# Kernel optimization log

Hardware: AMD Instinct MI355X
Metric: run time of the kernel (lower is better)

Reference implementation:

```python
import jax, jax.numpy as jnp
import numpy as np
from functools import partial

VOCAB = 32000
EMBED = 512
HIDDEN = 1024
NUM_LAYERS = 2
REP_PENALTY = 1.2
BATCH, SEQ = 64, 128


def _lstm_layer(xs, w_ih, w_hh, b_ih, b_hh):
    """PyTorch-convention LSTM layer. xs: [B,T,D_in] -> hs: [B,T,H].
    Gate order i,f,g,o; weights [4H, D_in]/[4H, H]."""
    B = xs.shape[0]
    H = w_hh.shape[1]
    # precompute input projections for all timesteps: [B,T,4H]
    x_proj = jnp.einsum('btd,gd->btg', xs, w_ih) + b_ih + b_hh

    def step(carry, xp):
        h, c = carry
        gates = xp + h @ w_hh.T  # [B,4H]
        i, f, g, o = jnp.split(gates, 4, axis=-1)
        i = jax.nn.sigmoid(i)
        f = jax.nn.sigmoid(f)
        g = jnp.tanh(g)
        o = jax.nn.sigmoid(o)
        c = f * c + i * g
        h = o * jnp.tanh(c)
        return (h, c), h

    h0 = jnp.zeros((B, H), xs.dtype)
    c0 = jnp.zeros((B, H), xs.dtype)
    _, hs = jax.lax.scan(step, (h0, c0), x_proj.transpose(1, 0, 2))  # [T,B,H]
    return hs.transpose(1, 0, 2)


def setup_inputs() -> dict:
    key = jax.random.key(0)
    ks = jax.random.split(key, 16)
    s_emb = 1.0  # nn.Embedding default init ~ N(0,1)
    x = jax.random.randint(ks[0], (BATCH, SEQ), 0, VOCAB, dtype=jnp.int32)
    emb = jax.random.normal(ks[1], (VOCAB, EMBED), jnp.float32) * s_emb

    def lstm_params(k, d_in):
        k1, k2, k3, k4 = jax.random.split(k, 4)
        s = 1.0 / np.sqrt(HIDDEN)
        return (
            jax.random.uniform(k1, (4 * HIDDEN, d_in), jnp.float32, -s, s),
            jax.random.uniform(k2, (4 * HIDDEN, HIDDEN), jnp.float32, -s, s),
            jax.random.uniform(k3, (4 * HIDDEN,), jnp.float32, -s, s),
            jax.random.uniform(k4, (4 * HIDDEN,), jnp.float32, -s, s),
        )

    w_ih0, w_hh0, b_ih0, b_hh0 = lstm_params(ks[2], EMBED)
    w_ih1, w_hh1, b_ih1, b_hh1 = lstm_params(ks[3], HIDDEN)
    s_fc = 1.0 / np.sqrt(HIDDEN)
    fc_w = jax.random.uniform(ks[4], (VOCAB, HIDDEN), jnp.float32, -s_fc, s_fc)
    fc_b = jax.random.uniform(ks[5], (VOCAB,), jnp.float32, -s_fc, s_fc)
    return {
        'x': x, 'emb': emb,
        'w_ih0': w_ih0, 'w_hh0': w_hh0, 'b_ih0': b_ih0, 'b_hh0': b_hh0,
        'w_ih1': w_ih1, 'w_hh1': w_hh1, 'b_ih1': b_ih1, 'b_hh1': b_hh1,
        'fc_w': fc_w, 'fc_b': fc_b,
    }


def reference(x, emb, w_ih0, w_hh0, b_ih0, b_hh0,
              w_ih1, w_hh1, b_ih1, b_hh1, fc_w, fc_b):
    h = emb[x]                                          # [B,S,E] embedding lookup
    h = _lstm_layer(h, w_ih0, w_hh0, b_ih0, b_hh0)      # [B,S,H]
    h = _lstm_layer(h, w_ih1, w_hh1, b_ih1, b_hh1)      # [B,S,H]
    last = h[:, -1, :]                                  # [B,H]
    out = last @ fc_w.T + fc_b                          # [B,V]
    # repetition penalty: each occurrence of token t in row i divides out[i,t]
    # by the penalty once => out[i,t] /= penalty**count(t in x[i]).
    B = x.shape[0]
    rows = jnp.broadcast_to(jnp.arange(B)[:, None], x.shape)
    counts = jnp.zeros((B, VOCAB), out.dtype).at[rows, x].add(1.0)
    out = out / jnp.power(jnp.asarray(REP_PENALTY, out.dtype), counts)
    return out
```

## Files before the change

kernel.cpp:

```cpp
#include <hip/hip_runtime.h>
#include <hip/hip_bf16.h>
#include <stdint.h>

#define NB 64
#define NT 128
#define NE 512
#define NH 1024
#define NV 32000
#define NM (NB*NT)

#define NWG 256
#define NTH 512
#define WPG 128
#define FLAG_STRIDE 32u

#define HS_SHORTS 32768u
#define GSTRIDE_SH (129u*HS_SHORTS)
#define WS_FLAGS_S 0u
#define WS_FLAGS_G 32768u
#define WS_H0      65536u
#define WS_H1      (WS_H0 + 2u*129u*65536u)
#define WS_CNT     (WS_H1 + 2u*129u*65536u)
#define WS_XS0     (WS_CNT + 4u*NB*NV)
#define WS_NEEDED  (WS_XS0 + 2u*NM*NE)

typedef __attribute__((ext_vector_type(8))) short bf16x8;
typedef __attribute__((ext_vector_type(4))) float f32x4;

#define SCOPE_AG  __HIP_MEMORY_SCOPE_AGENT

__device__ __forceinline__ unsigned short f2bf(float f) {
  unsigned u = __float_as_uint(f);
  u += 0x7FFFu + ((u >> 16) & 1u);
  return (unsigned short)(u >> 16);
}
__device__ __forceinline__ float sigmoidf_(float x) {
  return 1.0f / (1.0f + expf(-x));
}
__device__ __forceinline__ bf16x8 pack8(float4 a, float4 b) {
  bf16x8 v;
  v[0]=(short)f2bf(a.x); v[1]=(short)f2bf(a.y); v[2]=(short)f2bf(a.z); v[3]=(short)f2bf(a.w);
  v[4]=(short)f2bf(b.x); v[5]=(short)f2bf(b.y); v[6]=(short)f2bf(b.z); v[7]=(short)f2bf(b.w);
  return v;
}

#define MFMA(a,b,c) __builtin_amdgcn_mfma_f32_16x16x32_bf16((a),(b),(c),0,0,0)

__global__ void __launch_bounds__(NTH, 2)
lstm_all(const int* __restrict__ x, const float* __restrict__ emb,
         const float* __restrict__ w_ih0, const float* __restrict__ w_hh0,
         const float* __restrict__ b_ih0, const float* __restrict__ b_hh0,
         const float* __restrict__ w_ih1, const float* __restrict__ w_hh1,
         const float* __restrict__ b_ih1, const float* __restrict__ b_hh1,
         const float* __restrict__ fc_w, const float* __restrict__ fc_b,
         float* __restrict__ out, unsigned char* __restrict__ wsb)
{
  __shared__ unsigned short sWih1[2*32*64*8];
  __shared__ unsigned short sWhh0c1[32*64*8];
  __shared__ unsigned short sWhh1c1[32*64*8];
  __shared__ float sG0[32][32], sG1a[32][32], sG1b[32][32], sGih[32][32];
  __shared__ float sB0[32], sB1[32];
  __shared__ alignas(16) unsigned short sH0[32][8], sH1[32][8];

  const int wg  = blockIdx.x;
  const int tid = threadIdx.x;
  const int wave = tid >> 6, lane = tid & 63;
  const int lr = lane & 15, lq = lane >> 4;
  const int g  = wg >> 7;
  const int wgl = wg & 127;

  unsigned* flagsS = (unsigned*)(wsb + WS_FLAGS_S);
  unsigned* gf     = (unsigned*)(wsb + WS_FLAGS_G) + (unsigned)g*WPG*FLAG_STRIDE;
  unsigned short* h0g = (unsigned short*)(wsb + WS_H0) + (size_t)g*GSTRIDE_SH;
  unsigned short* h1g = (unsigned short*)(wsb + WS_H1) + (size_t)g*GSTRIDE_SH;
  unsigned* counts = (unsigned*)(wsb + WS_CNT);
  unsigned short* xs0 = (unsigned short*)(wsb + WS_XS0);

  bf16x8 breg[32];
  {
    const int ggr0 = (lr >> 3)*NH + wgl*8 + (lr & 7);
    const int ggr1 = (2 + (lr >> 3))*NH + wgl*8 + (lr & 7);
    if (wave == 2 || wave == 3) {
      const float* src = w_hh0 + (size_t)ggr0*NH + lq*8;
      #pragma unroll
      for (int kk = 0; kk < 32; ++kk)
        breg[kk] = pack8(*(const float4*)(src + kk*32), *(const float4*)(src + kk*32 + 4));
    } else if (wave == 0 || wave == 1) {
      const float* src = w_hh1 + (size_t)ggr0*NH + lq*8;
      #pragma unroll
      for (int kk = 0; kk < 32; ++kk)
        breg[kk] = pack8(*(const float4*)(src + kk*32), *(const float4*)(src + kk*32 + 4));
    } else if (wave == 4 || wave == 5) {
      const float* s0 = w_ih0 + (size_t)ggr0*NE + lq*8;
      const float* s1 = w_ih0 + (size_t)ggr1*NE + lq*8;
      #pragma unroll
      for (int kk = 0; kk < 16; ++kk) {
        breg[kk]    = pack8(*(const float4*)(s0 + kk*32), *(const float4*)(s0 + kk*32 + 4));
        breg[16+kk] = pack8(*(const float4*)(s1 + kk*32), *(const float4*)(s1 + kk*32 + 4));
      }
    }
  }

  for (int i = wg*NTH + tid; i < NM*(NE/8); i += NWG*NTH) {
    int m = i >> 6;
    int e8 = (i & 63) << 3;
    int t = m >> 6, b = m & 63;
    int tok = x[b*NT + t];
    const float* s = emb + (size_t)tok*NE + e8;
    union { bf16x8 v8; unsigned long long u[2]; } u;
    u.v8 = pack8(*(const float4*)s, *(const float4*)(s + 4));
    int gg = b >> 5, bb = b & 31;
    size_t off = ((size_t)((gg*NT + t)*2 + (bb >> 4)))*8192
               + ((size_t)((e8 >> 5)*64 + ((e8 >> 3) & 3)*16 + (bb & 15)))*8;
    unsigned long long* dst = (unsigned long long*)(xs0 + off);
    __hip_atomic_store(dst,   u.u[0], __ATOMIC_RELAXED, SCOPE_AG);
    __hip_atomic_store(dst+1, u.u[1], __ATOMIC_RELAXED, SCOPE_AG);
  }

  for (int i = tid; i < 2*32*64; i += NTH) {
    int ct = i >> 11, kk = (i >> 6) & 31, l = i & 63;
    int glr = l & 15, glq = l >> 4;
    int c = ct*16 + glr;
    int ggr = (c >> 3)*NH + wgl*8 + (c & 7);
    const float* p = w_ih1 + (size_t)ggr*NH + kk*32 + glq*8;
    ((bf16x8*)sWih1)[i] = pack8(*(const float4*)p, *(const float4*)(p + 4));
  }
  for (int i = tid; i < 32*64; i += NTH) {
    int kk = i >> 6, l = i & 63;
    int glr = l & 15, glq = l >> 4;
    int ggr = (2 + (glr >> 3))*NH + wgl*8 + (glr & 7);
    const float* p0 = w_hh0 + (size_t)ggr*NH + kk*32 + glq*8;
    const float* p1 = w_hh1 + (size_t)ggr*NH + kk*32 + glq*8;
    ((bf16x8*)sWhh0c1)[i] = pack8(*(const float4*)p0, *(const float4*)(p0 + 4));
    ((bf16x8*)sWhh1c1)[i] = pack8(*(const float4*)p1, *(const float4*)(p1 + 4));
  }
  if (tid < 32) {
    int g2 = (tid >> 3)*NH + wgl*8 + (tid & 7);
    sB0[tid] = b_ih0[g2] + b_hh0[g2];
    sB1[tid] = b_ih1[g2] + b_hh1[g2];
  }
  {
    int i = wg*NTH + tid;
    if (i < NB*NT) {
      int b = i >> 7;
      atomicAdd(&counts[(size_t)b*NV + x[i]], 1u);
    }
  }
  __syncthreads();
  if (tid == 0)
    __hip_atomic_store(&flagsS[(unsigned)wg * FLAG_STRIDE], 1u, __ATOMIC_RELAXED, SCOPE_AG);
  if (tid < NWG) {
    while (__hip_atomic_load(&flagsS[(unsigned)tid * FLAG_STRIDE], __ATOMIC_RELAXED, SCOPE_AG) < 1u)
      __builtin_amdgcn_s_sleep(8);
  }
  __syncthreads();

  float c_reg = 0.f;
  const int cbb = (tid & 255) >> 3, cu8 = tid & 7;
  for (int t = 0; t <= NT; ++t) {
    if (wave == 2 || wave == 3) {
      const int rb = wave - 2;
      const unsigned short* A = h0g + (size_t)t*HS_SHORTS + rb*16384 + lane*8;
      f32x4 a00 = {0.f,0.f,0.f,0.f}, a01 = {0.f,0.f,0.f,0.f};
      f32x4 a10 = {0.f,0.f,0.f,0.f}, a11 = {0.f,0.f,0.f,0.f};
      #pragma unroll
      for (int kk = 0; kk < 32; ++kk) {
        bf16x8 af = *(const bf16x8*)(A + kk*512);
        a00 = MFMA(af, breg[kk], a00);
        a01 = MFMA(af, ((const bf16x8*)sWhh0c1)[kk*64 + lane], a01);
        a10 = MFMA(af, ((const bf16x8*)sWih1)[kk*64 + lane], a10);
        a11 = MFMA(af, ((const bf16x8*)sWih1)[(32+kk)*64 + lane], a11);
      }
      #pragma unroll
      for (int r = 0; r < 4; ++r) {
        int row = rb*16 + lq*4 + r;
        sG0 [row][lr]    = a00[r];
        sG0 [row][16+lr] = a01[r];
        sG1a[row][lr]    = a10[r];
        sG1a[row][16+lr] = a11[r];
      }
    } else if (wave == 0 || wave == 1) {
      if (t >= 1) {
        const int rb = wave;
        const unsigned short* A = h1g + (size_t)(t-1)*HS_SHORTS + rb*16384 + lane*8;
        f32x4 a20 = {0.f,0.f,0.f,0.f}, a21 = {0.f,0.f,0.f,0.f};
        #pragma unroll
        for (int kk = 0; kk < 32; ++kk) {
          bf16x8 af = *(const bf16x8*)(A + kk*512);
          a20 = MFMA(af, breg[kk], a20);
          a21 = MFMA(af, ((const bf16x8*)sWhh1c1)[kk*64 + lane], a21);
        }
        #pragma unroll
        for (int r = 0; r < 4; ++r) {
          int row = rb*16 + lq*4 + r;
          sG1b[row][lr]    = a20[r];
          sG1b[row][16+lr] = a21[r];
        }
      }
    } else if (wave == 4 || wave == 5) {
      if (t < NT) {
        const int rb = wave - 4;
        const unsigned short* A = xs0 + ((size_t)((g*NT + t)*2 + rb))*8192 + lane*8;
        f32x4 ai0 = {0.f,0.f,0.f,0.f}, ai1 = {0.f,0.f,0.f,0.f};
        #pragma unroll
        for (int kk = 0; kk < 16; ++kk) {
          bf16x8 af = *(const bf16x8*)(A + kk*512);
          ai0 = MFMA(af, breg[kk], ai0);
          ai1 = MFMA(af, breg[16+kk], ai1);
        }
        #pragma unroll
        for (int r = 0; r < 4; ++r) {
          int row = rb*16 + lq*4 + r;
          sGih[row][lr]    = ai0[r];
          sGih[row][16+lr] = ai1[r];
        }
      }
    }
    __syncthreads();
    if (tid < 256) {
      if (t < NT) {
        float gi = sG0[cbb][cu8]    + sGih[cbb][cu8]    + sB0[cu8];
        float gf = sG0[cbb][8+cu8]  + sGih[cbb][8+cu8]  + sB0[8+cu8];
        float gg = sG0[cbb][16+cu8] + sGih[cbb][16+cu8] + sB0[16+cu8];
        float go = sG0[cbb][24+cu8] + sGih[cbb][24+cu8] + sB0[24+cu8];
        float ii = sigmoidf_(gi), ff = sigmoidf_(gf), gv = tanhf(gg), oo = sigmoidf_(go);
        c_reg = ff*c_reg + ii*gv;
        sH0[cbb][cu8] = f2bf(oo * tanhf(c_reg));
      }
    } else {
      if (t >= 1) {
        float gi = sG1a[cbb][cu8]    + sG1b[cbb][cu8]    + sB1[cu8];
        float gf = sG1a[cbb][8+cu8]  + sG1b[cbb][8+cu8]  + sB1[8+cu8];
        float gg = sG1a[cbb][16+cu8] + sG1b[cbb][16+cu8] + sB1[16+cu8];
        float go = sG1a[cbb][24+cu8] + sG1b[cbb][24+cu8] + sB1[24+cu8];
        float ii = sigmoidf_(gi), ff = sigmoidf_(gf), gv = tanhf(gg), oo = sigmoidf_(go);
        c_reg = ff*c_reg + ii*gv;
        sH1[cbb][cu8] = f2bf(oo * tanhf(c_reg));
      }
    }
    __syncthreads();
    if (wave == 6 && t < NT) {
      int bb = lane >> 1, j0 = (lane & 1)*4;
      unsigned long long v = *(const unsigned long long*)&sH0[bb][j0];
      size_t off = ((size_t)(((bb >> 4)*32 + (wgl >> 2))*64 + (wgl & 3)*16 + (bb & 15)))*8 + j0;
      __hip_atomic_store((unsigned long long*)(h0g + (size_t)(t+1)*HS_SHORTS + off),
                         v, __ATOMIC_RELAXED, SCOPE_AG);
    }
    if (wave == 7 && t >= 1) {
      int bb = lane >> 1, j0 = (lane & 1)*4;
      unsigned long long v = *(const unsigned long long*)&sH1[bb][j0];
      size_t off = ((size_t)(((bb >> 4)*32 + (wgl >> 2))*64 + (wgl & 3)*16 + (bb & 15)))*8 + j0;
      __hip_atomic_store((unsigned long long*)(h1g + (size_t)t*HS_SHORTS + off),
                         v, __ATOMIC_RELAXED, SCOPE_AG);
    }
    __syncthreads();
    if (tid == 0)
      __hip_atomic_store(&gf[(unsigned)wgl * FLAG_STRIDE], (unsigned)(t+1),
                         __ATOMIC_RELAXED, SCOPE_AG);
    if (tid < WPG) {
      while (__hip_atomic_load(&gf[(unsigned)tid * FLAG_STRIDE],
                               __ATOMIC_RELAXED, SCOPE_AG) < (unsigned)(t+1))
        __builtin_amdgcn_s_sleep(4);
    }
    __syncthreads();
  }

  {
    const unsigned short* ab = h1g + (size_t)128*HS_SHORTS + lane*8;
    for (int tile = wgl*8 + wave; tile < NV/16; tile += WPG*8) {
      int c0 = tile*16;
      const float* wb = fc_w + (size_t)(c0 + lr)*NH + lq*8;
      f32x4 acc0 = {0.f,0.f,0.f,0.f}, acc1 = {0.f,0.f,0.f,0.f};
      #pragma unroll 4
      for (int kk = 0; kk < 32; ++kk) {
        bf16x8 bfv = pack8(*(const float4*)(wb + kk*32), *(const float4*)(wb + kk*32 + 4));
        acc0 = MFMA(*(const bf16x8*)(ab + kk*512),         bfv, acc0);
        acc1 = MFMA(*(const bf16x8*)(ab + 16384 + kk*512), bfv, acc1);
      }
      int c = c0 + lr;
      float fb = fc_b[c];
      #pragma unroll
      for (int r = 0; r < 4; ++r) {
        int b0 = g*32 + lq*4 + r;
        int b1 = b0 + 16;
        unsigned cnt0 = counts[(size_t)b0*NV + c];
        unsigned cnt1 = counts[(size_t)b1*NV + c];
        out[(size_t)b0*NV + c] = (acc0[r] + fb) * exp2f(-0.26303440583379378f * (float)cnt0);
        out[(size_t)b1*NV + c] = (acc1[r] + fb) * exp2f(-0.26303440583379378f * (float)cnt1);
      }
    }
  }
}

extern "C" void kernel_launch(void* const* d_in, const int* in_sizes, int n_in,
                              void* d_out, int out_size, void* d_ws, size_t ws_size,
                              hipStream_t stream) {
  const int*   x     = (const int*)  d_in[0];
  const float* emb   = (const float*)d_in[1];
  const float* w_ih0 = (const float*)d_in[2];
  const float* w_hh0 = (const float*)d_in[3];
  const float* b_ih0 = (const float*)d_in[4];
  const float* b_hh0 = (const float*)d_in[5];
  const float* w_ih1 = (const float*)d_in[6];
  const float* w_hh1 = (const float*)d_in[7];
  const float* b_ih1 = (const float*)d_in[8];
  const float* b_hh1 = (const float*)d_in[9];
  const float* fc_w  = (const float*)d_in[10];
  const float* fc_b  = (const float*)d_in[11];
  if (ws_size < WS_NEEDED) return;
  unsigned char* ws = (unsigned char*)d_ws;
  (void)hipMemsetAsync(ws, 0, WS_H0, stream);
  (void)hipMemsetAsync(ws + WS_H0, 0, 65536, stream);
  (void)hipMemsetAsync(ws + WS_H0 + 129u*65536u, 0, 65536, stream);
  (void)hipMemsetAsync(ws + WS_H1, 0, 65536, stream);
  (void)hipMemsetAsync(ws + WS_H1 + 129u*65536u, 0, 65536, stream);
  (void)hipMemsetAsync(ws + WS_CNT, 0, 4u*NB*NV, stream);
  hipLaunchKernelGGL(lstm_all, dim3(NWG), dim3(NTH), 0, stream,
                     x, emb, w_ih0, w_hh0, b_ih0, b_hh0,
                     w_ih1, w_hh1, b_ih1, b_hh1, fc_w, fc_b,
                     (float*)d_out, (unsigned char*)d_ws);
}
```

Measured before the change: 991.3 us.

## Publish hidden state via shuffles, prefetch fc weights in idle waves, shorten spin sleep

The hidden-state publish now happens straight from the gate threads: wave shuffles pack eight bf16 values into two 64-bit atomic stores. This removes the shared-memory staging buffers and one __syncthreads per timestep. Idle waves 6 and 7 stream slices of fc_w during the recurrence to warm the cache for the final projection, kept alive by a dummy XOR accumulator. The flag-wait sleep is also reduced to poll more often. Together these shorten the serial per-step critical path and overlap the fc weight load with it, at the cost of extra memory traffic during the recurrence and more polling pressure.

```diff
diff --git a/kernel.cpp b/kernel.cpp
--- a/kernel.cpp
+++ b/kernel.cpp
@@ -18,7 +18,8 @@
 #define GSTRIDE_SH (129u*HS_SHORTS)
 #define WS_FLAGS_S 0u
 #define WS_FLAGS_G 32768u
-#define WS_H0      65536u
+#define WS_DUMP    65536u
+#define WS_H0      131072u
 #define WS_H1      (WS_H0 + 2u*129u*65536u)
 #define WS_CNT     (WS_H1 + 2u*129u*65536u)
 #define WS_XS0     (WS_CNT + 4u*NB*NV)
@@ -60,7 +61,6 @@
   __shared__ unsigned short sWhh1c1[32*64*8];
   __shared__ float sG0[32][32], sG1a[32][32], sG1b[32][32], sGih[32][32];
   __shared__ float sB0[32], sB1[32];
-  __shared__ alignas(16) unsigned short sH0[32][8], sH1[32][8];
 
   const int wg  = blockIdx.x;
   const int tid = threadIdx.x;
@@ -156,7 +156,9 @@
   __syncthreads();
 
   float c_reg = 0.f;
+  unsigned warmacc = 0;
   const int cbb = (tid & 255) >> 3, cu8 = tid & 7;
+  const size_t pub16 = ((size_t)(((cbb >> 4)*32 + (wgl >> 2))*64 + (wgl & 3)*16 + (cbb & 15)))*8;
   for (int t = 0; t <= NT; ++t) {
     if (wave == 2 || wave == 3) {
       const int rb = wave - 2;
@@ -215,6 +217,14 @@
           sGih[row][16+lr] = ai1[r];
         }
       }
+    } else {
+      size_t c = ((size_t)(t*2 + (wave-6))*NWG + wg)*64 + lane;
+      if (c*8 + 8 <= (size_t)NV*NH) {
+        float4 wv0 = *(const float4*)(fc_w + c*8);
+        float4 wv1 = *(const float4*)(fc_w + c*8 + 4);
+        warmacc ^= __float_as_uint(wv0.x) ^ __float_as_uint(wv0.w)
+                 ^ __float_as_uint(wv1.x) ^ __float_as_uint(wv1.w);
+      }
     }
     __syncthreads();
     if (tid < 256) {
@@ -225,7 +235,19 @@
         float go = sG0[cbb][24+cu8] + sGih[cbb][24+cu8] + sB0[24+cu8];
         float ii = sigmoidf_(gi), ff = sigmoidf_(gf), gv = tanhf(gg), oo = sigmoidf_(go);
         c_reg = ff*c_reg + ii*gv;
-        sH0[cbb][cu8] = f2bf(oo * tanhf(c_reg));
+        unsigned hb = f2bf(oo * tanhf(c_reg));
+        unsigned p0 = hb | (__shfl_down((int)hb, 1) << 16);
+        unsigned w1 = (unsigned)__shfl_down((int)p0, 2);
+        unsigned w2 = (unsigned)__shfl_down((int)p0, 4);
+        unsigned w3 = (unsigned)__shfl_down((int)w1, 4);
+        if (cu8 == 0) {
+          unsigned long long* dst =
+            (unsigned long long*)(h0g + (size_t)(t+1)*HS_SHORTS + pub16);
+          __hip_atomic_store(dst,   (unsigned long long)p0 | ((unsigned long long)w1 << 32),
+                             __ATOMIC_RELAXED, SCOPE_AG);
+          __hip_atomic_store(dst+1, (unsigned long long)w2 | ((unsigned long long)w3 << 32),
+                             __ATOMIC_RELAXED, SCOPE_AG);
+        }
       }
     } else {
       if (t >= 1) {
@@ -235,23 +257,20 @@
         float go = sG1a[cbb][24+cu8] + sG1b[cbb][24+cu8] + sB1[24+cu8];
         float ii = sigmoidf_(gi), ff = sigmoidf_(gf), gv = tanhf(gg), oo = sigmoidf_(go);
         c_reg = ff*c_reg + ii*gv;
-        sH1[cbb][cu8] = f2bf(oo * tanhf(c_reg));
-      }
-    }
-    __syncthreads();
-    if (wave == 6 && t < NT) {
-      int bb = lane >> 1, j0 = (lane & 1)*4;
-      unsigned long long v = *(const unsigned long long*)&sH0[bb][j0];
-      size_t off = ((size_t)(((bb >> 4)*32 + (wgl >> 2))*64 + (wgl & 3)*16 + (bb & 15)))*8 + j0;
-      __hip_atomic_store((unsigned long long*)(h0g + (size_t)(t+1)*HS_SHORTS + off),
-                         v, __ATOMIC_RELAXED, SCOPE_AG);
-    }
-    if (wave == 7 && t >= 1) {
-      int bb = lane >> 1, j0 = (lane & 1)*4;
-      unsigned long long v = *(const unsigned long long*)&sH1[bb][j0];
-      size_t off = ((size_t)(((bb >> 4)*32 + (wgl >> 2))*64 + (wgl & 3)*16 + (bb & 15)))*8 + j0;
-      __hip_atomic_store((unsigned long long*)(h1g + (size_t)t*HS_SHORTS + off),
-                         v, __ATOMIC_RELAXED, SCOPE_AG);
+        unsigned hb = f2bf(oo * tanhf(c_reg));
+        unsigned p0 = hb | (__shfl_down((int)hb, 1) << 16);
+        unsigned w1 = (unsigned)__shfl_down((int)p0, 2);
+        unsigned w2 = (unsigned)__shfl_down((int)p0, 4);
+        unsigned w3 = (unsigned)__shfl_down((int)w1, 4);
+        if (cu8 == 0) {
+          unsigned long long* dst =
+            (unsigned long long*)(h1g + (size_t)t*HS_SHORTS + pub16);
+          __hip_atomic_store(dst,   (unsigned long long)p0 | ((unsigned long long)w1 << 32),
+                             __ATOMIC_RELAXED, SCOPE_AG);
+          __hip_atomic_store(dst+1, (unsigned long long)w2 | ((unsigned long long)w3 << 32),
+                             __ATOMIC_RELAXED, SCOPE_AG);
+        }
+      }
     }
     __syncthreads();
     if (tid == 0)
@@ -260,7 +279,7 @@
     if (tid < WPG) {
       while (__hip_atomic_load(&gf[(unsigned)tid * FLAG_STRIDE],
                                __ATOMIC_RELAXED, SCOPE_AG) < (unsigned)(t+1))
-        __builtin_amdgcn_s_sleep(4);
+        __builtin_amdgcn_s_sleep(1);
     }
     __syncthreads();
   }
@@ -290,6 +309,8 @@
       }
     }
   }
+  if (warmacc == 0xDEADBEEFu)
+    ((volatile unsigned*)(wsb + WS_DUMP))[lane] = warmacc;
 }
 
 extern "C" void kernel_launch(void* const* d_in, const int* in_sizes, int n_in,
```

Result: no change. 0.9997 ms (+0.9%).

## Sync all workgroups before FC head and share fc_w loads across both batch halves

Applied to the files above, without the earlier changes.

Adds a grid-wide barrier after the recurrent loop so every workgroup can read the final hidden state of both batch groups. Each wave then computes one 16-column tile for all 64 batch rows, so each fc_w tile is loaded and converted to bf16 once instead of twice. This halves global traffic on the large FC weight matrix and spreads tiles over all 256 workgroups. The cost is an extra global barrier and more accumulator registers per wave.

```diff
diff --git a/kernel.cpp b/kernel.cpp
--- a/kernel.cpp
+++ b/kernel.cpp
@@ -265,28 +265,47 @@
     __syncthreads();
   }
 
+  if (tid == 0)
+    __hip_atomic_store(&flagsS[(unsigned)wg * FLAG_STRIDE], 2u, __ATOMIC_RELAXED, SCOPE_AG);
+  if (tid < NWG) {
+    while (__hip_atomic_load(&flagsS[(unsigned)tid * FLAG_STRIDE], __ATOMIC_RELAXED, SCOPE_AG) < 2u)
+      __builtin_amdgcn_s_sleep(4);
+  }
+  __syncthreads();
+
   {
-    const unsigned short* ab = h1g + (size_t)128*HS_SHORTS + lane*8;
-    for (int tile = wgl*8 + wave; tile < NV/16; tile += WPG*8) {
+    const unsigned short* ab0 = (unsigned short*)(wsb + WS_H1) + (size_t)128*HS_SHORTS + lane*8;
+    const unsigned short* ab1 = ab0 + GSTRIDE_SH;
+    int tile = wg*8 + wave;
+    if (tile < NV/16) {
       int c0 = tile*16;
       const float* wb = fc_w + (size_t)(c0 + lr)*NH + lq*8;
-      f32x4 acc0 = {0.f,0.f,0.f,0.f}, acc1 = {0.f,0.f,0.f,0.f};
+      f32x4 acc00 = {0.f,0.f,0.f,0.f}, acc01 = {0.f,0.f,0.f,0.f};
+      f32x4 acc10 = {0.f,0.f,0.f,0.f}, acc11 = {0.f,0.f,0.f,0.f};
       #pragma unroll 4
       for (int kk = 0; kk < 32; ++kk) {
         bf16x8 bfv = pack8(*(const float4*)(wb + kk*32), *(const float4*)(wb + kk*32 + 4));
-        acc0 = MFMA(*(const bf16x8*)(ab + kk*512),         bfv, acc0);
-        acc1 = MFMA(*(const bf16x8*)(ab + 16384 + kk*512), bfv, acc1);
+        acc00 = MFMA(*(const bf16x8*)(ab0 + kk*512),         bfv, acc00);
+        acc01 = MFMA(*(const bf16x8*)(ab0 + 16384 + kk*512), bfv, acc01);
+        acc10 = MFMA(*(const bf16x8*)(ab1 + kk*512),         bfv, acc10);
+        acc11 = MFMA(*(const bf16x8*)(ab1 + 16384 + kk*512), bfv, acc11);
       }
       int c = c0 + lr;
       float fb = fc_b[c];
       #pragma unroll
       for (int r = 0; r < 4; ++r) {
-        int b0 = g*32 + lq*4 + r;
-        int b1 = b0 + 16;
-        unsigned cnt0 = counts[(size_t)b0*NV + c];
-        unsigned cnt1 = counts[(size_t)b1*NV + c];
-        out[(size_t)b0*NV + c] = (acc0[r] + fb) * exp2f(-0.26303440583379378f * (float)cnt0);
-        out[(size_t)b1*NV + c] = (acc1[r] + fb) * exp2f(-0.26303440583379378f * (float)cnt1);
+        int b00 = lq*4 + r;
+        int b01 = b00 + 16;
+        int b10 = b00 + 32;
+        int b11 = b00 + 48;
+        unsigned cnt00 = counts[(size_t)b00*NV + c];
+        unsigned cnt01 = counts[(size_t)b01*NV + c];
+        unsigned cnt10 = counts[(size_t)b10*NV + c];
+        unsigned cnt11 = counts[(size_t)b11*NV + c];
+        out[(size_t)b00*NV + c] = (acc00[r] + fb) * exp2f(-0.26303440583379378f * (float)cnt00);
+        out[(size_t)b01*NV + c] = (acc01[r] + fb) * exp2f(-0.26303440583379378f * (float)cnt01);
+        out[(size_t)b10*NV + c] = (acc10[r] + fb) * exp2f(-0.26303440583379378f * (float)cnt10);
+        out[(size_t)b11*NV + c] = (acc11[r] + fb) * exp2f(-0.26303440583379378f * (float)cnt11);
       }
     }
   }
```

New measurement: 986.2 us. Within noise of the previous version (-0.5%).
